# Performance work log

Hardware: AMD Instinct MI355X
Metric: run time of the kernel (lower is better)

## Reference

```python
import jax, jax.numpy as jnp
import numpy as np

HIDDEN_DIM = 1024
NUM_HEADS = 16
HEAD_DIM = HIDDEN_DIM // NUM_HEADS


def setup_inputs() -> dict:
    key = jax.random.key(0)
    ks = jax.random.split(key, 9)
    s = 1.0 / np.sqrt(HIDDEN_DIM)
    x = jax.random.normal(ks[0], (2, 2048, HIDDEN_DIM), dtype=jnp.float32)
    Wq = jax.random.uniform(ks[1], (HIDDEN_DIM, HIDDEN_DIM), jnp.float32, -s, s)
    bq = jax.random.uniform(ks[2], (HIDDEN_DIM,), jnp.float32, -s, s)
    Wk = jax.random.uniform(ks[3], (HIDDEN_DIM, HIDDEN_DIM), jnp.float32, -s, s)
    bk = jax.random.uniform(ks[4], (HIDDEN_DIM,), jnp.float32, -s, s)
    Wv = jax.random.uniform(ks[5], (HIDDEN_DIM, HIDDEN_DIM), jnp.float32, -s, s)
    bv = jax.random.uniform(ks[6], (HIDDEN_DIM,), jnp.float32, -s, s)
    Wo = jax.random.uniform(ks[7], (HIDDEN_DIM, HIDDEN_DIM), jnp.float32, -s, s)
    bo = jax.random.uniform(ks[8], (HIDDEN_DIM,), jnp.float32, -s, s)
    return {"x": x, "Wq": Wq, "bq": bq, "Wk": Wk, "bk": bk,
            "Wv": Wv, "bv": bv, "Wo": Wo, "bo": bo}


def reference(x, Wq, bq, Wk, bk, Wv, bv, Wo, bo):
    B, M, D = x.shape
    H, Dh = NUM_HEADS, HEAD_DIM
    # projections -> [B, H, M, Dh]
    def split_heads(t):
        return t.reshape(B, M, H, Dh).transpose(0, 2, 1, 3)
    q = split_heads(x @ Wq.T + bq)
    k = split_heads(x @ Wk.T + bk)
    v = split_heads(x @ Wv.T + bv)
    scores = jnp.einsum('bhmd,bhnd->bhmn', q, k) / np.sqrt(Dh).astype(np.float32)
    # multiplicative diagonal-zero mask: zero the diagonal of the score matrix
    diag_zero = 1.0 - jnp.eye(M, dtype=scores.dtype)  # [M, M]
    scores = scores * diag_zero
    attn = jax.nn.softmax(scores, axis=-1)
    context = jnp.einsum('bhmn,bhnd->bhmd', attn, v)
    context = context.transpose(0, 2, 1, 3).reshape(B, M, D)
    return context @ Wo.T + bo
```

## Files before the change

kernel.cpp:

```cpp
#include <hip/hip_runtime.h>
#include <stdint.h>

typedef _Float16 f16;
typedef __attribute__((ext_vector_type(8))) _Float16 f16x8;
typedef __attribute__((ext_vector_type(4))) _Float16 f16x4;
typedef __attribute__((ext_vector_type(2))) __fp16 fp16x2;
typedef __attribute__((ext_vector_type(4))) float f32x4;

#define HD 1024
#define NH 16
#define DH 64
#define BB 2
#define MM 2048
#define BH (BB*NH)
#define MT (BB*MM)

__device__ __forceinline__ void gl_lds16(const f16* g, f16* l) {
    __builtin_amdgcn_global_load_lds((const __attribute__((address_space(1))) uint32_t*)g,
                                     (__attribute__((address_space(3))) uint32_t*)l, 16, 0, 0);
}

__device__ __forceinline__ float fexp2(float x) {
    float r; asm("v_exp_f32 %0, %1" : "=v"(r) : "v"(x)); return r;
}

__global__ void cvt_all(const float* __restrict__ x,  const float* __restrict__ wq,
                        const float* __restrict__ wk, const float* __restrict__ wv,
                        const float* __restrict__ wo, f16* __restrict__ dst) {
    const int XN4 = MT * HD / 4;
    const int WN4 = HD * HD / 4;
    int i = blockIdx.x * blockDim.x + threadIdx.x;
    if (i >= XN4 + 4 * WN4) return;
    const float* s; int off;
    if (i < XN4) { s = x; off = i; }
    else {
        int k = i - XN4, wsel = k >> 18;
        off = k & (WN4 - 1);
        s = wsel == 0 ? wq : wsel == 1 ? wk : wsel == 2 ? wv : wo;
    }
    float4 v = ((const float4*)s)[off];
    f16x4 h;
    h[0] = (f16)v.x; h[1] = (f16)v.y; h[2] = (f16)v.z; h[3] = (f16)v.w;
    ((f16x4*)dst)[i] = h;
}

template<int MODE>
__global__ __launch_bounds__(256, 3) void gemm_m97(const f16* __restrict__ A,
                                                   const f16* __restrict__ W,
                                                   const float* __restrict__ b0,
                                                   const float* __restrict__ b1,
                                                   const float* __restrict__ b2,
                                                   f16* __restrict__ oh,
                                                   float* __restrict__ of) {
    __shared__ f16 As[128 * 32];
    __shared__ f16 Bs[128 * 32];
    const int bid = blockIdx.x;
    int bn, bm;
    if (MODE == 0) { int xcd = bid & 7, r = bid >> 3; bn = xcd * 3 + (r >> 5); bm = r & 31; }
    else           { bn = bid & 7; bm = bid >> 3; }
    const int t = threadIdx.x, w = t >> 6, lane = t & 63;
    const int wr = w >> 1, wc = w & 1, lr = lane & 15, lg = lane >> 4;
    f32x4 acc[4][4] = {};

    const int srow = w * 16 + (lane >> 2);
    const int schunk = lane & 3;
    const f16* Ab = A + (size_t)(bm * 128) * HD;
    const f16* Wb = W + (size_t)(bn * 128) * HD;
    f16* Asw = As + w * 512;
    f16* Bsw = Bs + w * 512;

    #pragma unroll
    for (int i = 0; i < 2; i++) {
        int r = i * 64 + srow;
        int gc = ((schunk ^ ((r >> 1) & 3)) * 8);
        gl_lds16(Ab + (size_t)r * HD + gc, Asw + i * 2048);
        gl_lds16(Wb + (size_t)r * HD + gc, Bsw + i * 2048);
    }

    for (int k0 = 0;;) {
        __syncthreads();
        f16x8 af[4], bf[4];
        #pragma unroll
        for (int i = 0; i < 4; i++) {
            int ra = wr * 64 + i * 16 + lr;
            af[i] = *(const f16x8*)(As + ra * 32 + ((lg ^ ((ra >> 1) & 3)) * 8));
            int rb = wc * 64 + i * 16 + lr;
            bf[i] = *(const f16x8*)(Bs + rb * 32 + ((lg ^ ((rb >> 1) & 3)) * 8));
        }
        #pragma unroll
        for (int i = 0; i < 4; i++)
            #pragma unroll
            for (int j = 0; j < 4; j++)
                acc[i][j] = __builtin_amdgcn_mfma_f32_16x16x32_f16(af[i], bf[j], acc[i][j], 0, 0, 0);
        k0 += 32;
        if (k0 >= HD) break;
        __syncthreads();
        #pragma unroll
        for (int i = 0; i < 2; i++) {
            int r = i * 64 + srow;
            int gc = ((schunk ^ ((r >> 1) & 3)) * 8);
            gl_lds16(Ab + (size_t)r * HD + k0 + gc, Asw + i * 2048);
            gl_lds16(Wb + (size_t)r * HD + k0 + gc, Bsw + i * 2048);
        }
    }

    if (MODE == 0) {
        const int mat = bn >> 3;
        const float* bp = mat == 0 ? b0 : mat == 1 ? b1 : b2;
        f16* base = oh + (size_t)mat * BH * MM * DH;
        #pragma unroll
        for (int i = 0; i < 4; i++) {
            #pragma unroll
            for (int j = 0; j < 4; j++) {
                int n = bn * 128 + wc * 64 + j * 16 + lr;
                int nn = n & 1023, h = nn >> 6, dh = nn & 63;
                float bvv = bp[nn];
                int mg0 = bm * 128 + wr * 64 + i * 16 + lg * 4;
                int b = mg0 >> 11, mmr0 = mg0 & 2047;
                if (mat == 2) {
                    f16x4 o;
                    #pragma unroll
                    for (int r = 0; r < 4; r++) o[r] = (f16)(acc[i][j][r] + bvv);
                    *(f16x4*)(base + ((size_t)((b * NH + h) * DH + dh)) * MM + mmr0) = o;
                } else {
                    float sc = (mat == 0) ? 0.1803368801111204f : 1.0f;
                    #pragma unroll
                    for (int r = 0; r < 4; r++)
                        base[((size_t)((b * NH + h) * MM + mmr0 + r)) * DH + dh] =
                            (f16)((acc[i][j][r] + bvv) * sc);
                }
            }
        }
    } else {
        #pragma unroll
        for (int i = 0; i < 4; i++)
            #pragma unroll
            for (int j = 0; j < 4; j++) {
                int n = bn * 128 + wc * 64 + j * 16 + lr;
                float bvv = b0[n];
                #pragma unroll
                for (int r = 0; r < 4; r++) {
                    int mg = bm * 128 + wr * 64 + i * 16 + lg * 4 + r;
                    of[(size_t)mg * HD + n] = acc[i][j][r] + bvv;
                }
            }
    }
}

__global__ __launch_bounds__(256, 4) void attn_kernel(const f16* __restrict__ Q,
                                                      const f16* __restrict__ K,
                                                      const f16* __restrict__ Vt,
                                                      f16* __restrict__ ctx) {
    __shared__ f16 Kl[2][64][64];
    __shared__ f16 Vl[2][64][64];
    __shared__ f16 Pl[4][32][32];
    const int bid = blockIdx.x;
    const int xcd = bid & 7, idx = bid >> 3;
    const int bh = xcd * 4 + (idx >> 5);
    const int qblk = idx & 31;

    const int t = threadIdx.x, w = t >> 6, lane = t & 63;
    const int lr = lane & 15, lg = lane >> 4;
    const int wq = w >> 1, wkv = w & 1;
    const int q0B = qblk * 64 + wq * 32;
    const int kvb = wkv * 32;

    const f16* Qb = Q + (size_t)bh * MM * DH;
    const f16* Kb = K + (size_t)bh * MM * DH;
    const f16* Vb = Vt + (size_t)bh * DH * MM;

    const int srow = lane >> 3;
    const int sxc = ((lane & 7) ^ srow) * 8;
    const int lds_r = w * 16;

    f16x8 qfr[2][2];
    #pragma unroll
    for (int qf = 0; qf < 2; qf++)
        #pragma unroll
        for (int c = 0; c < 2; c++)
            qfr[qf][c] = *(const f16x8*)(Qb + (size_t)(q0B + qf * 16 + lr) * DH + c * 32 + lg * 8);

    f32x4 po[4][2] = {};
    float lsum0 = 0.f, lsum1 = 0.f;
    const int sw = (lr & 7) * 8;
    const int ko0 = (lg * 8) ^ sw, ko1 = (32 + lg * 8) ^ sw;
    const int vko = (kvb + lg * 8) ^ sw;
    const int ps = (lr >> 1) & 3;
    f16* Pw = &Pl[w][0][0];
    const int pro = lr * 32 + ((lg ^ ps) * 8);

    #pragma unroll
    for (int i = 0; i < 2; i++) {
        int row = lds_r + i * 8 + srow;
        gl_lds16(Kb + (size_t)row * DH + sxc, &Kl[0][lds_r + i * 8][0]);
        gl_lds16(Vb + (size_t)row * MM + sxc, &Vl[0][lds_r + i * 8][0]);
    }

#define ATTN_BODY(CUR, IT, VMN)                                                              \
    {                                                                                        \
        const int it_ = (IT);                                                                \
        if (it_ < 31) {                                                                      \
            const int jn = (it_ + 1) * 64;                                                   \
            _Pragma("unroll")                                                                \
            for (int i = 0; i < 2; i++) {                                                    \
                int row = lds_r + i * 8 + srow;                                              \
                gl_lds16(Kb + (size_t)(jn + row) * DH + sxc, &Kl[CUR ^ 1][lds_r + i * 8][0]);\
                gl_lds16(Vb + (size_t)row * MM + jn + sxc, &Vl[CUR ^ 1][lds_r + i * 8][0]); \
            }                                                                                \
        }                                                                                    \
        asm volatile("s_waitcnt vmcnt(" #VMN ")" ::: "memory");                              \
        __builtin_amdgcn_s_barrier();                                                        \
                        \
        f32x4 s00 = {}, s01 = {}, s10 = {}, s11 = {};                         \
        __builtin_amdgcn_s_setprio(1);                                                       \
        {                                                                                    \
            const f16* kr0 = &Kl[CUR][kvb + lr][0];                                          \
            f16x8 ka = *(const f16x8*)(kr0 + ko0);                                           \
            f16x8 kb = *(const f16x8*)(kr0 + ko1);                                           \
            s00 = __builtin_amdgcn_mfma_f32_16x16x32_f16(ka, qfr[0][0], s00, 0, 0, 0);       \
            s00 = __builtin_amdgcn_mfma_f32_16x16x32_f16(kb, qfr[0][1], s00, 0, 0, 0);       \
            s01 = __builtin_amdgcn_mfma_f32_16x16x32_f16(ka, qfr[1][0], s01, 0, 0, 0);       \
            s01 = __builtin_amdgcn_mfma_f32_16x16x32_f16(kb, qfr[1][1], s01, 0, 0, 0);       \
            const f16* kr1 = &Kl[CUR][kvb + 16 + lr][0];                                     \
            f16x8 kc = *(const f16x8*)(kr1 + ko0);                                           \
            f16x8 kd = *(const f16x8*)(kr1 + ko1);                                           \
            s10 = __builtin_amdgcn_mfma_f32_16x16x32_f16(kc, qfr[0][0], s10, 0, 0, 0);       \
            s10 = __builtin_amdgcn_mfma_f32_16x16x32_f16(kd, qfr[0][1], s10, 0, 0, 0);       \
            s11 = __builtin_amdgcn_mfma_f32_16x16x32_f16(kc, qfr[1][0], s11, 0, 0, 0);       \
            s11 = __builtin_amdgcn_mfma_f32_16x16x32_f16(kd, qfr[1][1], s11, 0, 0, 0);       \
        }                                                                                    \
        __builtin_amdgcn_s_setprio(0);                                                       \
                \
        if (it_ == qblk && wq == wkv) {                                                      \
            int rr = lr - lg * 4;                                                            \
            if (rr >= 0 && rr < 4) { s00[rr] = 0.f; s11[rr] = 0.f; }                         \
        }                                                                                    \
                  \
        _Pragma("unroll")                                                                    \
        for (int u = 0; u < 4; u++) {                                                        \
            const f32x4 sv = (u == 0) ? s00 : (u == 1) ? s01 : (u == 2) ? s10 : s11;         \
            const int fq = u >> 1, qf = u & 1;                                               \
            float p0 = fexp2(sv[0]), p1 = fexp2(sv[1]);                                      \
            float p2 = fexp2(sv[2]), p3 = fexp2(sv[3]);                                      \
            if (qf == 0) lsum0 += (p0 + p1) + (p2 + p3);                                     \
            else         lsum1 += (p0 + p1) + (p2 + p3);                                     \
            fp16x2 lo = __builtin_amdgcn_cvt_pkrtz(p0, p1);                                  \
            fp16x2 hi = __builtin_amdgcn_cvt_pkrtz(p2, p3);                                  \
            uint2 pr; pr.x = __builtin_bit_cast(uint32_t, lo);                               \
            pr.y = __builtin_bit_cast(uint32_t, hi);                                         \
            *(f16x4*)(Pw + (qf * 16 + lr) * 32 +                                             \
                      (((fq * 2 + (lg >> 1)) ^ ps) * 8) + (lg & 1) * 4) =                    \
                __builtin_bit_cast(f16x4, pr);                                               \
        }                                                                                    \
        asm volatile("s_waitcnt lgkmcnt(0)" ::: "memory");      \
        f16x8 pf0 = *(const f16x8*)(Pw + pro);                                               \
        f16x8 pf1 = *(const f16x8*)(Pw + 512 + pro);           \
                                             \
        __builtin_amdgcn_s_setprio(1);                                                       \
        _Pragma("unroll")                                                                    \
        for (int df = 0; df < 4; df++) {                                                     \
            const f16* vr = &Vl[CUR][df * 16 + lr][0];                                       \
            f16x8 va = *(const f16x8*)(vr + vko);                                            \
            po[df][0] = __builtin_amdgcn_mfma_f32_16x16x32_f16(va, pf0, po[df][0], 0, 0, 0); \
            po[df][1] = __builtin_amdgcn_mfma_f32_16x16x32_f16(va, pf1, po[df][1], 0, 0, 0); \
        }                                                                                    \
        __builtin_amdgcn_s_setprio(0);                                                       \
        asm volatile("" ::: "memory");                                                       \
        __builtin_amdgcn_s_barrier();                                                        \
    }

    for (int itp = 0; itp < 15; ++itp) {
        ATTN_BODY(0, 2 * itp, 4)
        ATTN_BODY(1, 2 * itp + 1, 4)
    }
    ATTN_BODY(0, 30, 4)
    ATTN_BODY(1, 31, 0)
#undef ATTN_BODY

    lsum0 += __shfl_xor(lsum0, 16); lsum0 += __shfl_xor(lsum0, 32);
    lsum1 += __shfl_xor(lsum1, 16); lsum1 += __shfl_xor(lsum1, 32);
    __syncthreads();
    float* shf0 = (float*)(&Kl[0][0][0]);
    float* shf1 = (float*)(&Vl[0][0][0]);
    float* shl  = (float*)(&Pl[0][0][0]);
    const int xi = wq * 64 + lane;
    if (wkv == 1) {
        float* d0 = shf0 + (size_t)xi * 17;
        float* d1 = shf1 + (size_t)xi * 17;
        #pragma unroll
        for (int df = 0; df < 4; df++) {
            *(f32x4*)(d0 + df * 4) = po[df][0];
            *(f32x4*)(d1 + df * 4) = po[df][1];
        }
        shl[xi * 2]     = lsum0;
        shl[xi * 2 + 1] = lsum1;
    }
    __syncthreads();
    if (wkv == 0) {
        const float* s0 = shf0 + (size_t)xi * 17;
        const float* s1 = shf1 + (size_t)xi * 17;
        const float inv0 = 1.f / (lsum0 + shl[xi * 2]);
        const float inv1 = 1.f / (lsum1 + shl[xi * 2 + 1]);
        const int b = bh >> 4, hh = bh & 15;
        #pragma unroll
        for (int qf = 0; qf < 2; qf++) {
            const float inv = qf ? inv1 : inv0;
            const float* s = qf ? s1 : s0;
            f16* cp = ctx + ((size_t)(b * MM + q0B + qf * 16 + lr)) * HD + hh * DH;
            #pragma unroll
            for (int df = 0; df < 4; df++) {
                f16x4 o;
                #pragma unroll
                for (int r = 0; r < 4; r++)
                    o[r] = (f16)((po[df][qf][r] + s[df * 4 + r]) * inv);
                *(f16x4*)(cp + df * 16 + lg * 4) = o;
            }
        }
    }
}

extern "C" void kernel_launch(void* const* d_in, const int* in_sizes, int n_in,
                              void* d_out, int out_size, void* d_ws, size_t ws_size,
                              hipStream_t stream) {
    const float* x  = (const float*)d_in[0];
    const float* Wq = (const float*)d_in[1];
    const float* bq = (const float*)d_in[2];
    const float* Wk = (const float*)d_in[3];
    const float* bk = (const float*)d_in[4];
    const float* Wv = (const float*)d_in[5];
    const float* bv = (const float*)d_in[6];
    const float* Wo = (const float*)d_in[7];
    const float* bo = (const float*)d_in[8];
    float* out = (float*)d_out;

    f16* xh  = (f16*)d_ws;
    f16* wqh = xh  + (size_t)MT * HD;
    f16* woh = wqh + (size_t)3 * HD * HD;
    f16* Qh  = woh + (size_t)HD * HD;
    f16* ctxh= Qh  + (size_t)3 * BH * MM * DH;

    const int total4 = MT * HD / 4 + HD * HD;
    cvt_all<<<(total4 + 255) / 256, 256, 0, stream>>>(x, Wq, Wk, Wv, Wo, xh);

    gemm_m97<0><<<768, 256, 0, stream>>>(xh, wqh, bq, bk, bv, Qh, nullptr);

    attn_kernel<<<1024, 256, 0, stream>>>(Qh, Qh + (size_t)BH * MM * DH,
                                          Qh + (size_t)2 * BH * MM * DH, ctxh);

    gemm_m97<1><<<256, 256, 0, stream>>>(ctxh, woh, bo, nullptr, nullptr, nullptr, out);
}
```

Baseline: 119.3 us.

## Triple-buffer K/V tiles in attention and use 512-thread blocks

The attention kernel now runs 8 waves per block covering 128 query rows, so each loaded K/V tile is shared by twice as many waves. K/V staging moves from a double to a triple LDS buffer, prefetching two tiles ahead. The trailing barrier in each iteration is dropped, leaving one barrier per KV tile. This cuts global/LDS load traffic per query and barrier count, but raises LDS per block to about 64KB, which may limit how many blocks fit on a CU.

```diff
diff --git a/kernel.cpp b/kernel.cpp
--- a/kernel.cpp
+++ b/kernel.cpp
@@ -147,31 +147,33 @@
     }
 }
 
-__global__ __launch_bounds__(256, 4) void attn_kernel(const f16* __restrict__ Q,
+__global__ __launch_bounds__(512, 4) void attn_kernel(const f16* __restrict__ Q,
                                                       const f16* __restrict__ K,
                                                       const f16* __restrict__ Vt,
                                                       f16* __restrict__ ctx) {
-    __shared__ f16 Kl[2][64][64];
-    __shared__ f16 Vl[2][64][64];
-    __shared__ f16 Pl[4][32][32];
+    __shared__ f16 Kl[3][64][64];
+    __shared__ f16 Vl[3][64][64];
+    __shared__ f16 Pl[8][32][32];
     const int bid = blockIdx.x;
     const int xcd = bid & 7, idx = bid >> 3;
-    const int bh = xcd * 4 + (idx >> 5);
-    const int qblk = idx & 31;
+    const int bh = xcd * 4 + (idx >> 4);
+    const int qblk2 = idx & 15;
 
     const int t = threadIdx.x, w = t >> 6, lane = t & 63;
     const int lr = lane & 15, lg = lane >> 4;
     const int wq = w >> 1, wkv = w & 1;
-    const int q0B = qblk * 64 + wq * 32;
+    const int q0B = qblk2 * 128 + wq * 32;
     const int kvb = wkv * 32;
+    const int dtile = q0B >> 6;
+    const bool dwave = (wkv == (wq & 1));
 
     const f16* Qb = Q + (size_t)bh * MM * DH;
     const f16* Kb = K + (size_t)bh * MM * DH;
     const f16* Vb = Vt + (size_t)bh * DH * MM;
 
-    const int srow = lane >> 3;
-    const int sxc = ((lane & 7) ^ srow) * 8;
-    const int lds_r = w * 16;
+    const int srowS = lane >> 3;
+    const int sxc = ((lane & 7) ^ srowS) * 8;
+    const int lds_r = w * 8;
 
     f16x8 qfr[2][2];
     #pragma unroll
@@ -190,27 +192,23 @@
     const int pro = lr * 32 + ((lg ^ ps) * 8);
 
     #pragma unroll
-    for (int i = 0; i < 2; i++) {
-        int row = lds_r + i * 8 + srow;
-        gl_lds16(Kb + (size_t)row * DH + sxc, &Kl[0][lds_r + i * 8][0]);
-        gl_lds16(Vb + (size_t)row * MM + sxc, &Vl[0][lds_r + i * 8][0]);
-    }
-
-#define ATTN_BODY(CUR, IT, VMN)                                                              \
+    for (int tt = 0; tt < 2; tt++) {
+        int row = lds_r + srowS;
+        gl_lds16(Kb + (size_t)(tt * 64 + row) * DH + sxc, &Kl[tt][lds_r][0]);
+        gl_lds16(Vb + (size_t)row * MM + tt * 64 + sxc, &Vl[tt][lds_r][0]);
+    }
+
+#define ATTN_BODY(CUR, NXT, IT, VMN)                                                         \
     {                                                                                        \
         const int it_ = (IT);                                                                \
-        if (it_ < 31) {                                                                      \
-            const int jn = (it_ + 1) * 64;                                                   \
-            _Pragma("unroll")                                                                \
-            for (int i = 0; i < 2; i++) {                                                    \
-                int row = lds_r + i * 8 + srow;                                              \
-                gl_lds16(Kb + (size_t)(jn + row) * DH + sxc, &Kl[CUR ^ 1][lds_r + i * 8][0]);\
-                gl_lds16(Vb + (size_t)row * MM + jn + sxc, &Vl[CUR ^ 1][lds_r + i * 8][0]); \
-            }                                                                                \
-        }                                                                                    \
-        asm volatile("s_waitcnt vmcnt(" #VMN ")" ::: "memory");                              \
-        __builtin_amdgcn_s_barrier();                                                        \
-                        \
+        asm volatile("s_waitcnt vmcnt(" #VMN ")" ::: "memory");    \
+        __builtin_amdgcn_s_barrier();                                  \
+        if (it_ < 30) {        \
+            const int jn = (it_ + 2) * 64;                                                   \
+            int row = lds_r + srowS;                                                         \
+            gl_lds16(Kb + (size_t)(jn + row) * DH + sxc, &Kl[NXT][lds_r][0]);                \
+            gl_lds16(Vb + (size_t)row * MM + jn + sxc, &Vl[NXT][lds_r][0]);                  \
+        }                                                                                    \
         f32x4 s00 = {}, s01 = {}, s10 = {}, s11 = {};                         \
         __builtin_amdgcn_s_setprio(1);                                                       \
         {                                                                                    \
@@ -230,12 +228,10 @@
             s11 = __builtin_amdgcn_mfma_f32_16x16x32_f16(kd, qfr[1][1], s11, 0, 0, 0);       \
         }                                                                                    \
         __builtin_amdgcn_s_setprio(0);                                                       \
-                \
-        if (it_ == qblk && wq == wkv) {                                                      \
+        if (it_ == dtile && dwave) {         \
             int rr = lr - lg * 4;                                                            \
             if (rr >= 0 && rr < 4) { s00[rr] = 0.f; s11[rr] = 0.f; }                         \
         }                                                                                    \
-                  \
         _Pragma("unroll")                                                                    \
         for (int u = 0; u < 4; u++) {                                                        \
             const f32x4 sv = (u == 0) ? s00 : (u == 1) ? s01 : (u == 2) ? s10 : s11;         \
@@ -254,8 +250,7 @@
         }                                                                                    \
         asm volatile("s_waitcnt lgkmcnt(0)" ::: "memory");      \
         f16x8 pf0 = *(const f16x8*)(Pw + pro);                                               \
-        f16x8 pf1 = *(const f16x8*)(Pw + 512 + pro);           \
-                                             \
+        f16x8 pf1 = *(const f16x8*)(Pw + 512 + pro);                                         \
         __builtin_amdgcn_s_setprio(1);                                                       \
         _Pragma("unroll")                                                                    \
         for (int df = 0; df < 4; df++) {                                                     \
@@ -265,16 +260,15 @@
             po[df][1] = __builtin_amdgcn_mfma_f32_16x16x32_f16(va, pf1, po[df][1], 0, 0, 0); \
         }                                                                                    \
         __builtin_amdgcn_s_setprio(0);                                                       \
-        asm volatile("" ::: "memory");                                                       \
-        __builtin_amdgcn_s_barrier();                                                        \
-    }
-
-    for (int itp = 0; itp < 15; ++itp) {
-        ATTN_BODY(0, 2 * itp, 4)
-        ATTN_BODY(1, 2 * itp + 1, 4)
-    }
-    ATTN_BODY(0, 30, 4)
-    ATTN_BODY(1, 31, 0)
+    }
+
+    for (int itp = 0; itp < 10; ++itp) {
+        ATTN_BODY(0, 2, 3 * itp,     2)
+        ATTN_BODY(1, 0, 3 * itp + 1, 2)
+        ATTN_BODY(2, 1, 3 * itp + 2, 2)
+    }
+    ATTN_BODY(0, 2, 30, 2)
+    ATTN_BODY(1, 0, 31, 0)
 #undef ATTN_BODY
 
     lsum0 += __shfl_xor(lsum0, 16); lsum0 += __shfl_xor(lsum0, 32);
@@ -344,8 +338,8 @@
 
     gemm_m97<0><<<768, 256, 0, stream>>>(xh, wqh, bq, bk, bv, Qh, nullptr);
 
-    attn_kernel<<<1024, 256, 0, stream>>>(Qh, Qh + (size_t)BH * MM * DH,
-                                          Qh + (size_t)2 * BH * MM * DH, ctxh);
+    attn_kernel<<<512, 512, 0, stream>>>(Qh, Qh + (size_t)BH * MM * DH,
+                                         Qh + (size_t)2 * BH * MM * DH, ctxh);
 
     gemm_m97<1><<<256, 256, 0, stream>>>(ctxh, woh, bo, nullptr, nullptr, nullptr, out);
 }
```

New measurement: 115.6 us. 3.1% less time.
